# Performance work log

Measured on AMD Instinct MI355X. Metric: run time of the kernel, lower is better.

## Reference

```python
import jax, jax.numpy as jnp
import numpy as np

B, T, C = 2, 2048, 1024
H, HS = 16, 64
THETA = 10000.0


def _rope_tables(seq_len, dim, dtype):
    inv_freq = 1.0 / (THETA ** (jnp.arange(0, dim, 2, dtype=jnp.float32) / dim))
    t = jnp.arange(seq_len, dtype=jnp.float32)
    freqs = t[:, None] * inv_freq[None, :]          # [T, dim/2]
    emb = jnp.concatenate([freqs, freqs], axis=-1)  # [T, dim]
    return jnp.cos(emb).astype(dtype), jnp.sin(emb).astype(dtype)


def _rotate_half(x):
    x1, x2 = jnp.split(x, 2, axis=-1)
    return jnp.concatenate([-x2, x1], axis=-1)


def setup_inputs() -> dict:
    key = jax.random.key(0)
    ks = jax.random.split(key, 9)
    s = 0.02
    return {
        "q_x": jax.random.normal(ks[0], (B, T, C), dtype=jnp.float32),
        "wq": jax.random.normal(ks[1], (C, H * HS), dtype=jnp.float32) * s,
        "bq": jnp.zeros((H * HS,), dtype=jnp.float32),
        "wk": jax.random.normal(ks[2], (C, H * HS), dtype=jnp.float32) * s,
        "bk": jnp.zeros((H * HS,), dtype=jnp.float32),
        "wv": jax.random.normal(ks[3], (C, H * HS), dtype=jnp.float32) * s,
        "bv": jnp.zeros((H * HS,), dtype=jnp.float32),
        "wc": jax.random.normal(ks[4], (H * HS, C), dtype=jnp.float32) * s,
        "bc": jnp.zeros((C,), dtype=jnp.float32),
    }


def reference(q_x, wq, bq, wk, bk, wv, bv, wc, bc):
    b, t, _ = q_x.shape
    # Q/K/V projections -> [B, H, T, HS]
    q = (q_x @ wq + bq).reshape(b, t, H, HS).transpose(0, 2, 1, 3)
    k = (q_x @ wk + bk).reshape(b, t, H, HS).transpose(0, 2, 1, 3)
    v = (q_x @ wv + bv).reshape(b, t, H, HS).transpose(0, 2, 1, 3)
    # RoPE (concat-half rotation)
    cos, sin = _rope_tables(t, HS, q.dtype)  # [T, HS]
    q = q * cos + _rotate_half(q) * sin
    k = k * cos + _rotate_half(k) * sin
    # Naive causal attention
    scale = 1.0 / np.sqrt(HS)
    att = jnp.einsum("bhqd,bhkd->bhqk", q, k) * scale
    mask = jnp.tril(jnp.ones((t, t), dtype=bool))
    att = jnp.where(mask, att, -jnp.inf)
    att = jax.nn.softmax(att, axis=-1)
    y = jnp.einsum("bhqk,bhkd->bhqd", att, v)
    y = y.transpose(0, 2, 1, 3).reshape(b, t, H * HS)
    return y @ wc + bc
```

## Files before the change

### kernel.cpp

```cpp
#include <hip/hip_runtime.h>

#define B_  2
#define T_  2048
#define C_  1024
#define H_  16
#define HS_ 64
#define M_  4096
#define N_  1024
#define K_  1024

typedef float floatx4 __attribute__((ext_vector_type(4)));
typedef short bf16x8  __attribute__((ext_vector_type(8)));

__device__ __forceinline__ float bf2f(unsigned short u) {
    return __uint_as_float(((unsigned int)u) << 16);
}
__device__ __forceinline__ unsigned short f2bf(float f) {
    unsigned int u = __float_as_uint(f);
    return (unsigned short)((u + 0x7fffu + ((u >> 16) & 1u)) >> 16);
}
__device__ __forceinline__ unsigned int pack2(float a, float b) {
    return (unsigned int)f2bf(a) | ((unsigned int)f2bf(b) << 16);
}
__device__ __forceinline__ void async16(const unsigned short* g, unsigned short* l) {
    __builtin_amdgcn_global_load_lds(
        (const __attribute__((address_space(1))) unsigned int*)g,
        (__attribute__((address_space(3))) unsigned int*)l, 16, 0, 0);
}

__global__ __launch_bounds__(256) void convert_x(const float* __restrict__ x,
                                                 unsigned short* __restrict__ xb)
{
    const size_t i = ((size_t)blockIdx.x * 256 + threadIdx.x) * 4;
    const float4 v = *(const float4*)(x + i);
    ushort4 st;
    st.x = f2bf(v.x); st.y = f2bf(v.y); st.z = f2bf(v.z); st.w = f2bf(v.w);
    *(ushort4*)(xb + i) = st;
}

__global__ __launch_bounds__(256) void transpose_w(
    const float* __restrict__ w0, const float* __restrict__ w1,
    const float* __restrict__ w2, const float* __restrict__ w3,
    unsigned short* __restrict__ wTall)
{
    __shared__ float tile[64][65];
    const int z = blockIdx.z;
    const float* w = (z == 0) ? w0 : (z == 1) ? w1 : (z == 2) ? w2 : w3;
    unsigned short* wT = wTall + ((size_t)z << 20);

    const int n0 = blockIdx.x * 64, k0 = blockIdx.y * 64;
    const int t = threadIdx.x;
    const int r = t >> 2, cq = (t & 3) * 16;

    const float4* src = (const float4*)(w + (size_t)(k0 + r) * N_ + n0 + cq);
    const float4 v0 = src[0], v1 = src[1], v2 = src[2], v3 = src[3];
    tile[r][cq+0]=v0.x; tile[r][cq+1]=v0.y; tile[r][cq+2]=v0.z; tile[r][cq+3]=v0.w;
    tile[r][cq+4]=v1.x; tile[r][cq+5]=v1.y; tile[r][cq+6]=v1.z; tile[r][cq+7]=v1.w;
    tile[r][cq+8]=v2.x; tile[r][cq+9]=v2.y; tile[r][cq+10]=v2.z; tile[r][cq+11]=v2.w;
    tile[r][cq+12]=v3.x; tile[r][cq+13]=v3.y; tile[r][cq+14]=v3.z; tile[r][cq+15]=v3.w;
    __syncthreads();

    const int rn = t >> 2, ck = (t & 3) * 16;
    unsigned int o[8];
#pragma unroll
    for (int ii = 0; ii < 8; ii++)
        o[ii] = pack2(tile[ck + 2*ii][rn], tile[ck + 2*ii + 1][rn]);
    unsigned short* dst = wT + (size_t)(n0 + rn) * K_ + k0 + ck;
    *(uint4*)dst       = make_uint4(o[0], o[1], o[2], o[3]);
    *(uint4*)(dst + 8) = make_uint4(o[4], o[5], o[6], o[7]);
}

__global__ __launch_bounds__(256) void qkv_gemm(
    const unsigned short* __restrict__ xb, const unsigned short* __restrict__ wT,
    const float* __restrict__ bq, const float* __restrict__ bk,
    const float* __restrict__ bv,
    unsigned short* __restrict__ qb, unsigned short* __restrict__ kb,
    unsigned short* __restrict__ vb)
{
    __shared__ unsigned short As[128 * 32];
    __shared__ unsigned short Bs[128 * 32];

    const int tid  = threadIdx.x;
    const int lane = tid & 63;
    const int wave = tid >> 6;
    const int p  = blockIdx.x >> 3;
    const int n0 = (blockIdx.x & 7) * 128;
    const int m0 = blockIdx.y * 128;
    const float* bias = (p == 0) ? bq : (p == 1) ? bk : bv;

    const int lrow = lane >> 2, lch = (lane & 3) * 8;
    const unsigned short* ag0 = xb + (size_t)(m0 + wave * 32 + lrow) * K_ + lch;
    const unsigned short* ag1 = ag0 + (size_t)16 * K_;
    const unsigned short* wb  = wT + ((size_t)p << 20);
    const unsigned short* bg0 = wb + (size_t)(n0 + wave * 32 + lrow) * K_ + lch;
    const unsigned short* bg1 = bg0 + (size_t)16 * K_;
    unsigned short* lA0 = &As[(wave * 32) * 32];
    unsigned short* lA1 = &As[(wave * 32 + 16) * 32];
    unsigned short* lB0 = &Bs[(wave * 32) * 32];
    unsigned short* lB1 = &Bs[(wave * 32 + 16) * 32];

    const int fr = lane & 15;
    const int fk = (lane >> 4) * 8;
    const int wr = wave >> 1, wc = wave & 1;

    floatx4 acc[4][4];
#pragma unroll
    for (int i = 0; i < 4; i++)
#pragma unroll
        for (int j = 0; j < 4; j++) acc[i][j] = (floatx4){0.f, 0.f, 0.f, 0.f};

    for (int k0 = 0; k0 < K_; k0 += 32) {
        __syncthreads();
        async16(ag0 + k0, lA0);
        async16(ag1 + k0, lA1);
        async16(bg0 + k0, lB0);
        async16(bg1 + k0, lB1);
        __syncthreads();

        bf16x8 af[4], bfr[4];
#pragma unroll
        for (int i = 0; i < 4; i++)
            af[i] = *(const bf16x8*)&As[(wr * 64 + i * 16 + fr) * 32 + fk];
#pragma unroll
        for (int j = 0; j < 4; j++)
            bfr[j] = *(const bf16x8*)&Bs[(wc * 64 + j * 16 + fr) * 32 + fk];
#pragma unroll
        for (int i = 0; i < 4; i++)
#pragma unroll
            for (int j = 0; j < 4; j++)
                acc[i][j] = __builtin_amdgcn_mfma_f32_16x16x32_bf16(
                    af[i], bfr[j], acc[i][j], 0, 0, 0);
    }

    const int rbase = (lane >> 4) * 4;
    const int h = (n0 + wc * 64) >> 6;
    if (p == 2) {
#pragma unroll
        for (int j = 0; j < 4; j++) {
            const int col = n0 + wc * 64 + j * 16 + fr;
            const float bz = bias[col];
            const int d = col & 63;
#pragma unroll
            for (int i = 0; i < 4; i++) {
                const int row0 = m0 + wr * 64 + i * 16 + rbase;
                const int bb = row0 >> 11, tt = row0 & 2047;
                ushort4 st;
                st.x = f2bf(acc[i][j][0] + bz);
                st.y = f2bf(acc[i][j][1] + bz);
                st.z = f2bf(acc[i][j][2] + bz);
                st.w = f2bf(acc[i][j][3] + bz);
                *(ushort4*)&vb[((size_t)(bb * H_ + h) * HS_ + d) * T_ + tt] = st;
            }
        }
    } else {
        unsigned short* out = (p == 0) ? qb : kb;
        const float qsc = (p == 0) ? 0.18033688011111772f : 1.0f;
        const float bz0 = bias[n0 + wc * 64 + fr];
        const float bz1 = bias[n0 + wc * 64 + 16 + fr];
        const float bz2 = bias[n0 + wc * 64 + 32 + fr];
        const float bz3 = bias[n0 + wc * 64 + 48 + fr];
        const float nl = -0.41524101186279297f;
        const float if0 = exp2f((float)fr * nl);
        const float if1 = exp2f((float)(fr + 16) * nl);
#pragma unroll
        for (int i = 0; i < 4; i++) {
#pragma unroll
            for (int pr = 0; pr < 4; pr++) {
                const int row = m0 + wr * 64 + i * 16 + rbase + pr;
                const int bb = row >> 11, tt = row & 2047;
                float s0, c0, s1, c1;
                __sincosf((float)tt * if0, &s0, &c0);
                __sincosf((float)tt * if1, &s1, &c1);
                const float v0 = acc[i][0][pr] + bz0;
                const float v1 = acc[i][1][pr] + bz1;
                const float v2 = acc[i][2][pr] + bz2;
                const float v3 = acc[i][3][pr] + bz3;
                unsigned short* ob = out + ((size_t)(bb * H_ + h) * T_ + tt) * HS_ + fr;
                ob[0]  = f2bf((v0 * c0 - v2 * s0) * qsc);
                ob[16] = f2bf((v1 * c1 - v3 * s1) * qsc);
                ob[32] = f2bf((v2 * c0 + v0 * s0) * qsc);
                ob[48] = f2bf((v3 * c1 + v1 * s1) * qsc);
            }
        }
    }
}

__global__ __launch_bounds__(256) void attn_kernel(
    const unsigned short* __restrict__ qb, const unsigned short* __restrict__ kb,
    const unsigned short* __restrict__ vt, unsigned short* __restrict__ yb)
{
    __shared__ unsigned short Ks[2][64 * 64];
    __shared__ unsigned short Vs[2][64 * 64];
    __shared__ unsigned short Ps[4][16 * 64];

    const int bh = blockIdx.x;
    const int b = bh >> 4, h = bh & 15;
    const int qt = (int)gridDim.y - 1 - blockIdx.y;
    const int r0 = qt * 64;
    const int tid  = threadIdx.x;
    const int lane = tid & 63;
    const int wave = tid >> 6;
    const int l4   = lane & 15;
    const int quad = lane >> 4;

    const int qrow_g = r0 + wave * 16 + l4;

    bf16x8 qf[2];
    {
        const unsigned short* qp = qb + ((size_t)bh * T_ + qrow_g) * HS_ + quad * 8;
        qf[0] = *(const bf16x8*)(qp);
        qf[1] = *(const bf16x8*)(qp + 32);
    }

    floatx4 o[4];
#pragma unroll
    for (int g = 0; g < 4; g++) o[g] = (floatx4){0.f, 0.f, 0.f, 0.f};
    float m = -1e30f, l = 0.f;

    const int srow = tid >> 2;
    const int sc16 = (tid & 3) * 16;
    const int ssw  = (srow & 7) * 8;
    const int psw  = (l4 & 7) * 8;

    const unsigned short* kp = kb + ((size_t)bh * T_ + srow) * HS_ + sc16;
    const unsigned short* vp = vt + ((size_t)(bh * 64 + srow)) * T_ + sc16;

    uint4 rk0 = *(const uint4*)kp;
    uint4 rk1 = *(const uint4*)(kp + 8);
    uint4 rv0 = *(const uint4*)vp;
    uint4 rv1 = *(const uint4*)(vp + 8);
    *(uint4*)&Ks[0][srow * 64 + ( sc16      ^ ssw)] = rk0;
    *(uint4*)&Ks[0][srow * 64 + ((sc16 + 8) ^ ssw)] = rk1;
    *(uint4*)&Vs[0][srow * 64 + ( sc16      ^ ssw)] = rv0;
    *(uint4*)&Vs[0][srow * 64 + ((sc16 + 8) ^ ssw)] = rv1;

    for (int kt = 0; kt <= qt; kt++) {
        const int cur = kt & 1;
        if (kt < qt) {
            const unsigned short* kpn = kp + (size_t)(kt + 1) * (64 * HS_);
            const unsigned short* vpn = vp + (kt + 1) * 64;
            rk0 = *(const uint4*)kpn;
            rk1 = *(const uint4*)(kpn + 8);
            rv0 = *(const uint4*)vpn;
            rv1 = *(const uint4*)(vpn + 8);
        }
        __syncthreads();

        floatx4 sf[4];
#pragma unroll
        for (int mg = 0; mg < 4; mg++) {
            const int key = mg * 16 + l4;
            const int ksw = (key & 7) * 8;
            const bf16x8 a0 = *(const bf16x8*)&Ks[cur][key * 64 + ( (quad * 8)       ^ ksw)];
            const bf16x8 a1 = *(const bf16x8*)&Ks[cur][key * 64 + (((quad * 8) + 32) ^ ksw)];
            floatx4 z = (floatx4){0.f, 0.f, 0.f, 0.f};
            z = __builtin_amdgcn_mfma_f32_16x16x32_bf16(a0, qf[0], z, 0, 0, 0);
            z = __builtin_amdgcn_mfma_f32_16x16x32_bf16(a1, qf[1], z, 0, 0, 0);
            sf[mg] = z;
        }

        if (kt == qt) {
#pragma unroll
            for (int mg = 0; mg < 4; mg++)
#pragma unroll
                for (int r = 0; r < 4; r++)
                    if (kt * 64 + 16 * mg + quad * 4 + r > qrow_g)
                        sf[mg][r] = -1e30f;
        }

        float tm = sf[0][0];
#pragma unroll
        for (int mg = 0; mg < 4; mg++)
#pragma unroll
            for (int r = 0; r < 4; r++) tm = fmaxf(tm, sf[mg][r]);
        tm = fmaxf(tm, __shfl_xor(tm, 16));
        tm = fmaxf(tm, __shfl_xor(tm, 32));
        const float mnew  = fmaxf(m, tm);
        const float alpha = exp2f(m - mnew);

        float p[4][4];
        float ps = 0.f;
#pragma unroll
        for (int mg = 0; mg < 4; mg++)
#pragma unroll
            for (int r = 0; r < 4; r++) {
                p[mg][r] = exp2f(sf[mg][r] - mnew);
                ps += p[mg][r];
            }
        ps += __shfl_xor(ps, 16);
        ps += __shfl_xor(ps, 32);
        l = l * alpha + ps;
        m = mnew;
#pragma unroll
        for (int g = 0; g < 4; g++) {
            o[g][0] *= alpha; o[g][1] *= alpha;
            o[g][2] *= alpha; o[g][3] *= alpha;
        }

#pragma unroll
        for (int mg = 0; mg < 4; mg++) {
            const int kb4 = 16 * mg + quad * 4;
            const int off = ((kb4 & ~7) ^ psw) | (kb4 & 7);
            uint2 w;
            w.x = pack2(p[mg][0], p[mg][1]);
            w.y = pack2(p[mg][2], p[mg][3]);
            *(uint2*)&Ps[wave][l4 * 64 + off] = w;
        }

        const bf16x8 pf0 = *(const bf16x8*)&Ps[wave][l4 * 64 + ( (quad * 8)       ^ psw)];
        const bf16x8 pf1 = *(const bf16x8*)&Ps[wave][l4 * 64 + (((quad * 8) + 32) ^ psw)];
#pragma unroll
        for (int g = 0; g < 4; g++) {
            const int vd  = g * 16 + l4;
            const int vsw = (vd & 7) * 8;
            const bf16x8 va0 = *(const bf16x8*)&Vs[cur][vd * 64 + ( (quad * 8)       ^ vsw)];
            const bf16x8 va1 = *(const bf16x8*)&Vs[cur][vd * 64 + (((quad * 8) + 32) ^ vsw)];
            o[g] = __builtin_amdgcn_mfma_f32_16x16x32_bf16(va0, pf0, o[g], 0, 0, 0);
            o[g] = __builtin_amdgcn_mfma_f32_16x16x32_bf16(va1, pf1, o[g], 0, 0, 0);
        }

        if (kt < qt) {
            const int nxt = cur ^ 1;
            *(uint4*)&Ks[nxt][srow * 64 + ( sc16      ^ ssw)] = rk0;
            *(uint4*)&Ks[nxt][srow * 64 + ((sc16 + 8) ^ ssw)] = rk1;
            *(uint4*)&Vs[nxt][srow * 64 + ( sc16      ^ ssw)] = rv0;
            *(uint4*)&Vs[nxt][srow * 64 + ((sc16 + 8) ^ ssw)] = rv1;
        }
    }

    const float invl = 1.f / l;
    unsigned short* yrow = yb + ((size_t)(b * T_ + qrow_g) * H_ + h) * HS_;
#pragma unroll
    for (int g = 0; g < 4; g++) {
        ushort4 st;
        st.x = f2bf(o[g][0] * invl);
        st.y = f2bf(o[g][1] * invl);
        st.z = f2bf(o[g][2] * invl);
        st.w = f2bf(o[g][3] * invl);
        *(ushort4*)&yrow[16 * g + quad * 4] = st;
    }
}

__global__ __launch_bounds__(256) void out_gemm(
    const unsigned short* __restrict__ A, const unsigned short* __restrict__ wcT,
    const float* __restrict__ bias, float* __restrict__ out)
{
    __shared__ unsigned short As[128 * 32];
    __shared__ unsigned short Bs[128 * 32];

    const int tid  = threadIdx.x;
    const int lane = tid & 63;
    const int wave = tid >> 6;
    const int n0 = blockIdx.x * 128;
    const int m0 = blockIdx.y * 128;

    const int lrow = lane >> 2, lch = (lane & 3) * 8;
    const unsigned short* ag0 = A + (size_t)(m0 + wave * 32 + lrow) * K_ + lch;
    const unsigned short* ag1 = ag0 + (size_t)16 * K_;
    const unsigned short* bg0 = wcT + (size_t)(n0 + wave * 32 + lrow) * K_ + lch;
    const unsigned short* bg1 = bg0 + (size_t)16 * K_;
    unsigned short* lA0 = &As[(wave * 32) * 32];
    unsigned short* lA1 = &As[(wave * 32 + 16) * 32];
    unsigned short* lB0 = &Bs[(wave * 32) * 32];
    unsigned short* lB1 = &Bs[(wave * 32 + 16) * 32];

    const int fr = lane & 15;
    const int fk = (lane >> 4) * 8;
    const int wr = wave >> 1, wc = wave & 1;

    floatx4 acc[4][4];
#pragma unroll
    for (int i = 0; i < 4; i++)
#pragma unroll
        for (int j = 0; j < 4; j++) acc[i][j] = (floatx4){0.f, 0.f, 0.f, 0.f};

    for (int k0 = 0; k0 < K_; k0 += 32) {
        __syncthreads();
        async16(ag0 + k0, lA0);
        async16(ag1 + k0, lA1);
        async16(bg0 + k0, lB0);
        async16(bg1 + k0, lB1);
        __syncthreads();

        bf16x8 af[4], bfr[4];
#pragma unroll
        for (int i = 0; i < 4; i++)
            af[i] = *(const bf16x8*)&As[(wr * 64 + i * 16 + fr) * 32 + fk];
#pragma unroll
        for (int j = 0; j < 4; j++)
            bfr[j] = *(const bf16x8*)&Bs[(wc * 64 + j * 16 + fr) * 32 + fk];
#pragma unroll
        for (int i = 0; i < 4; i++)
#pragma unroll
            for (int j = 0; j < 4; j++)
                acc[i][j] = __builtin_amdgcn_mfma_f32_16x16x32_bf16(
                    af[i], bfr[j], acc[i][j], 0, 0, 0);
    }

    const int rbase = (lane >> 4) * 4;
#pragma unroll
    for (int j = 0; j < 4; j++) {
        const int col = n0 + wc * 64 + j * 16 + fr;
        const float bz = bias[col];
#pragma unroll
        for (int i = 0; i < 4; i++) {
#pragma unroll
            for (int pr = 0; pr < 4; pr++) {
                const int row = m0 + wr * 64 + i * 16 + rbase + pr;
                out[(size_t)row * N_ + col] = acc[i][j][pr] + bz;
            }
        }
    }
}

extern "C" void kernel_launch(void* const* d_in, const int* in_sizes, int n_in,
                              void* d_out, int out_size, void* d_ws, size_t ws_size,
                              hipStream_t stream) {
    const float* x  = (const float*)d_in[0];
    const float* wq = (const float*)d_in[1];
    const float* bq = (const float*)d_in[2];
    const float* wk = (const float*)d_in[3];
    const float* bk = (const float*)d_in[4];
    const float* wv = (const float*)d_in[5];
    const float* bv = (const float*)d_in[6];
    const float* wc = (const float*)d_in[7];
    const float* bc = (const float*)d_in[8];
    float* out = (float*)d_out;

    unsigned short* ws  = (unsigned short*)d_ws;
    unsigned short* qb  = ws;
    unsigned short* kb  = ws + (size_t)4194304;
    unsigned short* vb  = ws + (size_t)8388608;
    unsigned short* yb  = ws + (size_t)12582912;
    unsigned short* xb  = ws + (size_t)16777216;
    unsigned short* wT  = ws + (size_t)20971520;
    unsigned short* wcT = wT + ((size_t)3 << 20);

    convert_x<<<4096, 256, 0, stream>>>(x, xb);
    transpose_w<<<dim3(16, 16, 4), 256, 0, stream>>>(wq, wk, wv, wc, wT);
    qkv_gemm<<<dim3(24, 32), 256, 0, stream>>>(xb, wT, bq, bk, bv, qb, kb, vb);
    attn_kernel<<<dim3(32, 32), 256, 0, stream>>>(qb, kb, vb, yb);
    out_gemm<<<dim3(8, 32), 256, 0, stream>>>(yb, wcT, bc, out);
}
```

Measured before the change: 215.3 us.

## Split long causal query tiles across two blocks and merge partial softmax results

Query tiles 16–31, which carry the longest causal key ranges, are each split into two blocks that cover half of the key tiles. Each half writes unnormalized bf16 partial outputs plus its row max and sum; a new combine kernel rescales and merges the two halves into y. This shortens the critical path and evens out per-block work, at the cost of an extra launch and partial-output traffic. Scratch buffers reuse workspace regions that are dead by then. The change also uses the hardware exp2 builtin and packs P to bf16 by truncation instead of rounding, trading a little accuracy for fewer instructions.

```diff
diff --git a/kernel.cpp b/kernel.cpp
--- a/kernel.cpp
+++ b/kernel.cpp
@@ -21,6 +21,9 @@
 }
 __device__ __forceinline__ unsigned int pack2(float a, float b) {
     return (unsigned int)f2bf(a) | ((unsigned int)f2bf(b) << 16);
+}
+__device__ __forceinline__ unsigned int pack2t(float a, float b) {
+    return __builtin_amdgcn_perm(__float_as_uint(b), __float_as_uint(a), 0x07060302u);
 }
 __device__ __forceinline__ void async16(const unsigned short* g, unsigned short* l) {
     __builtin_amdgcn_global_load_lds(
@@ -187,7 +190,8 @@
 
 __global__ __launch_bounds__(256) void attn_kernel(
     const unsigned short* __restrict__ qb, const unsigned short* __restrict__ kb,
-    const unsigned short* __restrict__ vt, unsigned short* __restrict__ yb)
+    const unsigned short* __restrict__ vt, unsigned short* __restrict__ yb,
+    unsigned short* __restrict__ Opart, float* __restrict__ Mpart)
 {
     __shared__ unsigned short Ks[2][64 * 64];
     __shared__ unsigned short Vs[2][64 * 64];
@@ -195,7 +199,18 @@
 
     const int bh = blockIdx.x;
     const int b = bh >> 4, h = bh & 15;
-    const int qt = (int)gridDim.y - 1 - blockIdx.y;
+    const int s = 47 - (int)blockIdx.y;
+    int qt, ktlo, kthi, half;
+    bool split;
+    if (s < 16) { qt = s; ktlo = 0; kthi = qt; half = 0; split = false; }
+    else {
+        const int idx = s - 16;
+        qt = 16 + (idx >> 1); half = idx & 1;
+        const int nf = (qt + 2) >> 1;
+        ktlo = half ? nf : 0;
+        kthi = half ? qt : nf - 1;
+        split = true;
+    }
     const int r0 = qt * 64;
     const int tid  = threadIdx.x;
     const int lane = tid & 63;
@@ -225,18 +240,18 @@
     const unsigned short* kp = kb + ((size_t)bh * T_ + srow) * HS_ + sc16;
     const unsigned short* vp = vt + ((size_t)(bh * 64 + srow)) * T_ + sc16;
 
-    uint4 rk0 = *(const uint4*)kp;
-    uint4 rk1 = *(const uint4*)(kp + 8);
-    uint4 rv0 = *(const uint4*)vp;
-    uint4 rv1 = *(const uint4*)(vp + 8);
+    uint4 rk0 = *(const uint4*)(kp + (size_t)ktlo * 64 * HS_);
+    uint4 rk1 = *(const uint4*)(kp + (size_t)ktlo * 64 * HS_ + 8);
+    uint4 rv0 = *(const uint4*)(vp + ktlo * 64);
+    uint4 rv1 = *(const uint4*)(vp + ktlo * 64 + 8);
     *(uint4*)&Ks[0][srow * 64 + ( sc16      ^ ssw)] = rk0;
     *(uint4*)&Ks[0][srow * 64 + ((sc16 + 8) ^ ssw)] = rk1;
     *(uint4*)&Vs[0][srow * 64 + ( sc16      ^ ssw)] = rv0;
     *(uint4*)&Vs[0][srow * 64 + ((sc16 + 8) ^ ssw)] = rv1;
 
-    for (int kt = 0; kt <= qt; kt++) {
-        const int cur = kt & 1;
-        if (kt < qt) {
+    for (int kt = ktlo; kt <= kthi; kt++) {
+        const int cur = (kt - ktlo) & 1;
+        if (kt < kthi) {
             const unsigned short* kpn = kp + (size_t)(kt + 1) * (64 * HS_);
             const unsigned short* vpn = vp + (kt + 1) * 64;
             rk0 = *(const uint4*)kpn;
@@ -276,7 +291,7 @@
         tm = fmaxf(tm, __shfl_xor(tm, 16));
         tm = fmaxf(tm, __shfl_xor(tm, 32));
         const float mnew  = fmaxf(m, tm);
-        const float alpha = exp2f(m - mnew);
+        const float alpha = __builtin_amdgcn_exp2f(m - mnew);
 
         float p[4][4];
         float ps = 0.f;
@@ -284,7 +299,7 @@
         for (int mg = 0; mg < 4; mg++)
 #pragma unroll
             for (int r = 0; r < 4; r++) {
-                p[mg][r] = exp2f(sf[mg][r] - mnew);
+                p[mg][r] = __builtin_amdgcn_exp2f(sf[mg][r] - mnew);
                 ps += p[mg][r];
             }
         ps += __shfl_xor(ps, 16);
@@ -292,18 +307,15 @@
         l = l * alpha + ps;
         m = mnew;
 #pragma unroll
-        for (int g = 0; g < 4; g++) {
-            o[g][0] *= alpha; o[g][1] *= alpha;
-            o[g][2] *= alpha; o[g][3] *= alpha;
-        }
+        for (int g = 0; g < 4; g++) o[g] = o[g] * alpha;
 
 #pragma unroll
         for (int mg = 0; mg < 4; mg++) {
             const int kb4 = 16 * mg + quad * 4;
             const int off = ((kb4 & ~7) ^ psw) | (kb4 & 7);
             uint2 w;
-            w.x = pack2(p[mg][0], p[mg][1]);
-            w.y = pack2(p[mg][2], p[mg][3]);
+            w.x = pack2t(p[mg][0], p[mg][1]);
+            w.y = pack2t(p[mg][2], p[mg][3]);
             *(uint2*)&Ps[wave][l4 * 64 + off] = w;
         }
 
@@ -319,7 +331,7 @@
             o[g] = __builtin_amdgcn_mfma_f32_16x16x32_bf16(va1, pf1, o[g], 0, 0, 0);
         }
 
-        if (kt < qt) {
+        if (kt < kthi) {
             const int nxt = cur ^ 1;
             *(uint4*)&Ks[nxt][srow * 64 + ( sc16      ^ ssw)] = rk0;
             *(uint4*)&Ks[nxt][srow * 64 + ((sc16 + 8) ^ ssw)] = rk1;
@@ -328,16 +340,79 @@
         }
     }
 
-    const float invl = 1.f / l;
-    unsigned short* yrow = yb + ((size_t)(b * T_ + qrow_g) * H_ + h) * HS_;
-#pragma unroll
-    for (int g = 0; g < 4; g++) {
-        ushort4 st;
-        st.x = f2bf(o[g][0] * invl);
-        st.y = f2bf(o[g][1] * invl);
-        st.z = f2bf(o[g][2] * invl);
-        st.w = f2bf(o[g][3] * invl);
-        *(ushort4*)&yrow[16 * g + quad * 4] = st;
+    if (!split) {
+        const float invl = 1.f / l;
+        unsigned short* yrow = yb + ((size_t)(b * T_ + qrow_g) * H_ + h) * HS_;
+#pragma unroll
+        for (int g = 0; g < 4; g++) {
+            ushort4 st;
+            st.x = f2bf(o[g][0] * invl);
+            st.y = f2bf(o[g][1] * invl);
+            st.z = f2bf(o[g][2] * invl);
+            st.w = f2bf(o[g][3] * invl);
+            *(ushort4*)&yrow[16 * g + quad * 4] = st;
+        }
+    } else {
+        const int u  = (bh * 16 + (qt - 16)) * 2 + half;
+        const int rl = wave * 16 + l4;
+        unsigned short* Op = Opart + (size_t)u * 4096 + rl * 64;
+#pragma unroll
+        for (int g = 0; g < 4; g++) {
+            ushort4 st;
+            st.x = f2bf(o[g][0]);
+            st.y = f2bf(o[g][1]);
+            st.z = f2bf(o[g][2]);
+            st.w = f2bf(o[g][3]);
+            *(ushort4*)&Op[16 * g + quad * 4] = st;
+        }
+        if (quad == 0) {
+            float* ml = Mpart + (size_t)u * 128;
+            ml[rl]      = m;
+            ml[64 + rl] = l;
+        }
+    }
+}
+
+__global__ __launch_bounds__(256) void attn_combine(
+    const unsigned short* __restrict__ Opart, const float* __restrict__ Mpart,
+    unsigned short* __restrict__ yb)
+{
+    const int u  = blockIdx.x;
+    const int bh = u >> 4, qt = 16 + (u & 15);
+    const int b = bh >> 4, h = bh & 15;
+    const int t = threadIdx.x;
+    const int r = t >> 2, c = (t & 3) * 16;
+
+    const float* ml1 = Mpart + (size_t)(u * 2) * 128;
+    const float* ml2 = ml1 + 128;
+    const float m1 = ml1[r], l1 = ml1[64 + r];
+    const float m2 = ml2[r], l2 = ml2[64 + r];
+    const float M  = fmaxf(m1, m2);
+    const float w1 = __builtin_amdgcn_exp2f(m1 - M);
+    const float w2 = __builtin_amdgcn_exp2f(m2 - M);
+    const float inv = 1.f / (l1 * w1 + l2 * w2);
+    const float a1 = w1 * inv, a2 = w2 * inv;
+
+    const unsigned short* O1 = Opart + (size_t)(u * 2)     * 4096 + r * 64 + c;
+    const unsigned short* O2 = Opart + (size_t)(u * 2 + 1) * 4096 + r * 64 + c;
+    unsigned short* yrow = yb + ((size_t)(b * T_ + qt * 64 + r) * H_ + h) * HS_ + c;
+
+#pragma unroll
+    for (int j = 0; j < 2; j++) {
+        const uint4 u1 = *(const uint4*)(O1 + 8 * j);
+        const uint4 u2 = *(const uint4*)(O2 + 8 * j);
+        const unsigned int a[4] = {u1.x, u1.y, u1.z, u1.w};
+        const unsigned int d[4] = {u2.x, u2.y, u2.z, u2.w};
+        unsigned int ov[4];
+#pragma unroll
+        for (int q = 0; q < 4; q++) {
+            const float y0 = bf2f((unsigned short)(a[q] & 0xffff)) * a1
+                           + bf2f((unsigned short)(d[q] & 0xffff)) * a2;
+            const float y1 = bf2f((unsigned short)(a[q] >> 16)) * a1
+                           + bf2f((unsigned short)(d[q] >> 16)) * a2;
+            ov[q] = pack2(y0, y1);
+        }
+        *(uint4*)(yrow + 8 * j) = make_uint4(ov[0], ov[1], ov[2], ov[3]);
     }
 }
 
@@ -435,10 +510,13 @@
     unsigned short* xb  = ws + (size_t)16777216;
     unsigned short* wT  = ws + (size_t)20971520;
     unsigned short* wcT = wT + ((size_t)3 << 20);
+    unsigned short* Opart = xb;
+    float*          Mpart = (float*)wT;
 
     convert_x<<<4096, 256, 0, stream>>>(x, xb);
     transpose_w<<<dim3(16, 16, 4), 256, 0, stream>>>(wq, wk, wv, wc, wT);
     qkv_gemm<<<dim3(24, 32), 256, 0, stream>>>(xb, wT, bq, bk, bv, qb, kb, vb);
-    attn_kernel<<<dim3(32, 32), 256, 0, stream>>>(qb, kb, vb, yb);
+    attn_kernel<<<dim3(32, 48), 256, 0, stream>>>(qb, kb, vb, yb, Opart, Mpart);
+    attn_combine<<<512, 256, 0, stream>>>(Opart, Mpart, yb);
     out_gemm<<<dim3(8, 32), 256, 0, stream>>>(yb, wcT, bc, out);
 }
```

New measurement: 211.1 us. No clear change (-1.9%).
